# Performance work log

Hardware: AMD Instinct MI355X
Metric: run time of the kernel (lower is better)

## Reference

```python
import jax, jax.numpy as jnp
import numpy as np

MOLS = 64
ATOMS = 256
N = MOLS * ATOMS
K_GB = 32
K_GNN = 16
HID = 128
OFFSET = 0.009            # GB dielectric offset (nm)
ALPHA, BETA, GAMMA = 1.0, 0.8, 4.85  # OBC2 coefficients
EPS_FACTOR = 138.935456   # Coulomb constant, kJ*nm/(mol*e^2)
PREF = -EPS_FACTOR * (1.0 - 1.0 / 78.5)


def _edges(key, k_neigh):
    # random intra-molecule neighbors, no self loops (mimics radius-graph structure)
    src = jnp.repeat(jnp.arange(N), k_neigh)
    off = jax.random.randint(key, (N * k_neigh,), 1, ATOMS)
    dst = (src // ATOMS) * ATOMS + (src % ATOMS + off) % ATOMS
    return jnp.stack([src, dst]).astype(jnp.int32)


def setup_inputs() -> dict:
    key = jax.random.key(0)
    ks = jax.random.split(key, 8)
    pos = (jax.random.uniform(ks[0], (N, 3), jnp.float32) * 1.5)
    q = jax.random.uniform(ks[1], (N, 1), jnp.float32) - 0.5
    rad = 0.15 + 0.05 * jax.random.uniform(ks[2], (N, 1), jnp.float32)
    scl = 0.8 + 0.2 * jax.random.uniform(ks[3], (N, 1), jnp.float32)
    rest = jax.random.uniform(ks[4], (N, 4), jnp.float32)
    atom_features = jnp.concatenate([q, rad, scl, rest], axis=1)
    batch = jnp.repeat(jnp.arange(MOLS), ATOMS).astype(jnp.int32)
    edge_index = _edges(ks[5], K_GB)
    gnn_edge_index = _edges(ks[6], K_GNN)

    def lin(k, fi, fo):
        return (jax.random.normal(k, (fi, fo), jnp.float32) / np.float32(np.sqrt(fi)),
                jnp.zeros((fo,), jnp.float32))
    kw = jax.random.split(ks[7], 6)
    i1_w1, i1_b1 = lin(kw[0], 2 * 2 + 1, HID)
    i1_w2, i1_b2 = lin(kw[1], HID, HID)
    i2_w1, i2_b1 = lin(kw[2], 2 * HID + 1, HID)
    i2_w2, i2_b2 = lin(kw[3], HID, HID)
    i3_w1, i3_b1 = lin(kw[4], 2 * HID + 1, HID)
    i3_w2, i3_b2 = lin(kw[5], HID, 1)
    return dict(pos=pos, atom_features=atom_features, batch=batch,
                edge_index=edge_index, gnn_edge_index=gnn_edge_index,
                i1_w1=i1_w1, i1_b1=i1_b1, i1_w2=i1_w2, i1_b2=i1_b2,
                i2_w1=i2_w1, i2_b1=i2_b1, i2_w2=i2_w2, i2_b2=i2_b2,
                i3_w1=i3_w1, i3_b1=i3_b1, i3_w2=i3_w2, i3_b2=i3_b2)


def _dist(pos, ei):
    d2 = jnp.sum((pos[ei[0]] - pos[ei[1]]) ** 2, axis=1)
    return jnp.sqrt(d2 + 1e-12)


def _gb_energies(pos, feats, ei):
    # GBNeck_interaction (Born radii via HCT descreening integral, OBC2 rescale)
    # followed by GBNeck_energies (pairwise GB + self energy), per-atom [N,1]
    n = pos.shape[0]
    src, dst = ei[0], ei[1]
    d = _dist(pos, ei)
    q, radius, scale = feats[:, 0], feats[:, 1], feats[:, 2]
    rho = radius - OFFSET
    sr_j = (scale * rho)[src]
    rho_i = rho[dst]
    U = d + sr_j
    L = jnp.maximum(rho_i, jnp.abs(d - sr_j))
    I = 0.5 * (1.0 / L - 1.0 / U
               + 0.25 * (d - sr_j ** 2 / d) * (1.0 / U ** 2 - 1.0 / L ** 2)
               + 0.5 * jnp.log(L / U) / d)
    I = jnp.where(rho_i < U, I, 0.0)
    Isum = jax.ops.segment_sum(I, dst, num_segments=n)
    psi = Isum * rho
    B = 1.0 / (1.0 / rho - jnp.tanh(ALPHA * psi - BETA * psi ** 2 + GAMMA * psi ** 3) / radius)
    Bi, Bj = B[dst], B[src]
    f_gb = jnp.sqrt(d ** 2 + Bi * Bj * jnp.exp(-d ** 2 / (4.0 * Bi * Bj)))
    e_pair = 0.5 * PREF * q[dst] * q[src] / f_gb  # 0.5: edges are double counted
    e = 0.5 * PREF * q ** 2 / B + jax.ops.segment_sum(e_pair, dst, num_segments=n)
    return e[:, None]


def _in_layer(x, ei, d, w1, b1, w2, b2):
    # IN_layer_all_swish_2pass: edge MLP on [x_i || x_j || d] + scatter-add
    n = x.shape[0]
    m = jnp.concatenate([x[ei[0]], x[ei[1]], d[:, None]], axis=1)
    h = jax.nn.silu(m @ w1 + b1)
    return jax.ops.segment_sum(h @ w2 + b2, ei[1], num_segments=n)


def _energies_all(pos, feats, ei, gei,
                  i1_w1, i1_b1, i1_w2, i1_b2,
                  i2_w1, i2_b1, i2_w2, i2_b2,
                  i3_w1, i3_b1, i3_w2, i3_b2):
    e_gb = _gb_energies(pos, feats, ei)
    d_gnn = _dist(pos, gei)
    x = jax.nn.silu(_in_layer(feats[:, :2], gei, d_gnn, i1_w1, i1_b1, i1_w2, i1_b2))
    x = jax.nn.silu(_in_layer(x, gei, d_gnn, i2_w1, i2_b1, i2_w2, i2_b2))
    x = _in_layer(x, gei, d_gnn, i3_w1, i3_b1, i3_w2, i3_b2)
    return e_gb + x


def reference(pos, atom_features, batch, edge_index, gnn_edge_index,
              i1_w1, i1_b1, i1_w2, i1_b2,
              i2_w1, i2_b1, i2_w2, i2_b2,
              i3_w1, i3_b1, i3_w2, i3_b2):
    ws = (i1_w1, i1_b1, i1_w2, i1_b2, i2_w1, i2_b1, i2_w2, i2_b2,
          i3_w1, i3_b1, i3_w2, i3_b2)
    efun = lambda p: _energies_all(p, atom_features, edge_index, gnn_edge_index, *ws)
    energies, vjp = jax.vjp(efun, pos)  # [N,1]
    (gpos,) = vjp(jnp.ones_like(energies))
    forces = -gpos
    energy = jax.ops.segment_sum(energies[:, 0], batch, num_segments=MOLS)[:, None]
    return energy, forces
```

## Files before the change

### kernel.cpp

```cpp
#include <hip/hip_runtime.h>
#include <hip/hip_bf16.h>

#define NATOMS 16384
#define MOLS   64
#define ATOMSM 256
#define EGB    524288
#define EGNN   262144
#define HID    128
#define NH     (NATOMS*HID)

#define OFFSETC 0.009f
#define ALPHAC  1.0f
#define BETAC   0.8f
#define GAMMAC  4.85f
#define PREFC   (-138.935456f*(1.0f-1.0f/78.5f))

typedef __hip_bfloat16 bf;
typedef __attribute__((ext_vector_type(8))) short bf8v;
typedef __attribute__((ext_vector_type(4))) float f4v;

__device__ __forceinline__ float b2f(bf x){ return __bfloat162float(x); }
__device__ __forceinline__ bf f2b(float x){ return __float2bfloat16(x); }
__device__ __forceinline__ short f2s(float x){ bf h = f2b(x); return *(short*)&h; }
__device__ __forceinline__ float s2f(short s){
    unsigned int x = ((unsigned int)(unsigned short)s) << 16;
    return __uint_as_float(x);
}
__device__ __forceinline__ float sigf(float x){ return 1.0f/(1.0f+__expf(-x)); }
__device__ __forceinline__ float waveRed(float v){
    v += __shfl_xor(v,32); v += __shfl_xor(v,16); v += __shfl_xor(v,8);
    v += __shfl_xor(v,4);  v += __shfl_xor(v,2);  v += __shfl_xor(v,1);
    return v;
}

__global__ __launch_bounds__(256) void k_gbA_dist(
    const float* __restrict__ pos, const float* __restrict__ feat,
    const int* __restrict__ ei, float* __restrict__ Isum,
    const int* __restrict__ gei, float* __restrict__ dgnn, int* __restrict__ cnt)
{
    int tid = threadIdx.x;
    if (blockIdx.x < 512){
        __shared__ float sPx[256], sPy[256], sPz[256], sRho[256], sSr[256];
        __shared__ float sI[256];
        int mbase = (blockIdx.x >> 3) * 256;
        {
            int i = mbase + tid;
            sPx[tid]=pos[3*i]; sPy[tid]=pos[3*i+1]; sPz[tid]=pos[3*i+2];
            float rad = feat[7*i+1], sc = feat[7*i+2];
            float rho = rad - OFFSETC;
            sRho[tid]=rho; sSr[tid]=sc*rho;
            sI[tid]=0.f;
        }
        __syncthreads();
        int T = blockIdx.x*256 + tid;
        int s = T >> 3, p = T & 7;
        int sl = s & 255;
        int e0 = s*32 + p*4;
        float px = sPx[sl], py = sPy[sl], pz = sPz[sl];
        float sr = sSr[sl];
        const int* dP = ei + EGB;
#pragma unroll
        for (int j=0;j<4;j++){
            int dl = dP[e0+j] & 255;
            float dx = px - sPx[dl];
            float dy = py - sPy[dl];
            float dz = pz - sPz[dl];
            float d  = sqrtf(dx*dx+dy*dy+dz*dz + 1e-12f);
            float rho_i = sRho[dl];
            float U = d + sr;
            if (rho_i < U){
                float L = fmaxf(rho_i, fabsf(d - sr));
                float invU = 1.0f/U, invL = 1.0f/L;
                float I = 0.5f*invL - 0.5f*invU
                        + 0.125f*(d - sr*sr/d)*(invU*invU - invL*invL)
                        + 0.25f*__logf(L*invU)/d;
                atomicAdd(&sI[dl], I);
            }
        }
        __syncthreads();
        atomicAdd(&Isum[mbase + tid], sI[tid]);
    } else {
        int e = (blockIdx.x-512)*256 + tid;
        if (e >= EGNN) return;
        int s = gei[e], dd = gei[EGNN+e];
        float dx = pos[3*s+0] - pos[3*dd+0];
        float dy = pos[3*s+1] - pos[3*dd+1];
        float dz = pos[3*s+2] - pos[3*dd+2];
        dgnn[e] = sqrtf(dx*dx+dy*dy+dz*dz + 1e-12f);
        atomicAdd(&cnt[dd], 1);
    }
}

__global__ __launch_bounds__(256) void k_gbB_scan(
    const float* __restrict__ feat, const float* __restrict__ Isum,
    float* __restrict__ Bv, float* __restrict__ cB, float* __restrict__ gB,
    float* __restrict__ egb,
    const int* __restrict__ cnt, int* __restrict__ rptr, int* __restrict__ cursor)
{
    int t = threadIdx.x;
    if (blockIdx.x < 64){
        int i = blockIdx.x*256 + t;
        float q   = feat[7*i+0];
        float rad = feat[7*i+1];
        float rho = rad - OFFSETC;
        float psi = Isum[i]*rho;
        float u = psi*(ALPHAC + psi*(-BETAC + GAMMAC*psi));
        float tt = tanhf(u);
        float B = 1.0f/(1.0f/rho - tt/rad);
        Bv[i] = B;
        float du = ALPHAC + psi*(-2.0f*BETAC + 3.0f*GAMMAC*psi);
        cB[i] = B*B*((1.0f-tt*tt)/rad)*du*rho;
        float Cs = 0.5f*PREFC*q*q;
        egb[i] = Cs/B;
        gB[i]  = -Cs/(B*B);
    } else {
        __shared__ int sc[256];
        int m = blockIdx.x - 64;
        int c = cnt[m*256+t];
        sc[t] = c; __syncthreads();
        for (int off=1; off<256; off<<=1){
            int x = (t>=off) ? sc[t-off] : 0;
            __syncthreads();
            sc[t] += x;
            __syncthreads();
        }
        int ex = m*4096 + sc[t] - c;
        rptr[m*256+t] = ex;
        cursor[m*256+t] = ex;
    }
}

__global__ __launch_bounds__(256) void k_gbC(
    const float* __restrict__ pos, const float* __restrict__ feat,
    const int* __restrict__ ei, const float* __restrict__ Bv,
    float* __restrict__ egb, float* __restrict__ gdgb, float* __restrict__ gB)
{
    __shared__ float sPx[256], sPy[256], sPz[256], sB[256], sQf[256];
    __shared__ float sE[256], sG[256];
    int tid = threadIdx.x;
    int mbase = (blockIdx.x >> 3) * 256;
    {
        int i = mbase + tid;
        sPx[tid]=pos[3*i]; sPy[tid]=pos[3*i+1]; sPz[tid]=pos[3*i+2];
        sB[tid]=Bv[i]; sQf[tid]=feat[7*i+0];
        sE[tid]=0.f; sG[tid]=0.f;
    }
    __syncthreads();
    int T = blockIdx.x*256 + tid;
    int s = T >> 3, p = T & 7;
    int sl = s & 255;
    int e0 = s*32 + p*4;
    float px = sPx[sl], py = sPy[sl], pz = sPz[sl];
    float qs = sQf[sl];
    float Bs = sB[sl];
    float gsrc = 0.f;
    const int* dP = ei + EGB;
#pragma unroll
    for (int j=0;j<4;j++){
        int dl = dP[e0+j] & 255;
        float dx = px - sPx[dl];
        float dy = py - sPy[dl];
        float dz = pz - sPz[dl];
        float d2 = dx*dx+dy*dy+dz*dz + 1e-12f;
        float d  = sqrtf(d2);
        float Bd = sB[dl];
        float C = 0.5f*PREFC*sQf[dl]*qs;
        float P = Bd*Bs;
        float ex = __expf(-d2/(4.f*P));
        float f2 = d2 + P*ex;
        float f  = sqrtf(f2);
        float f3i = 1.f/(f2*f);
        gdgb[e0+j] = -C*d*(1.f - 0.25f*ex)*f3i;
        float common = -C*ex*(1.f + d2/(4.f*P))*0.5f*f3i;
        atomicAdd(&sE[dl], C/f);
        atomicAdd(&sG[dl], common*Bs);
        gsrc += common*Bd;
    }
    gsrc += __shfl_xor(gsrc,1);
    gsrc += __shfl_xor(gsrc,2);
    gsrc += __shfl_xor(gsrc,4);
    if (p==0) atomicAdd(&sG[sl], gsrc);
    __syncthreads();
    atomicAdd(&egb[mbase + tid], sE[tid]);
    atomicAdd(&gB[mbase + tid],  sG[tid]);
}

__global__ __launch_bounds__(256) void k_gbE(
    const float* __restrict__ pos, const float* __restrict__ feat,
    const int* __restrict__ ei, const float* __restrict__ cB,
    const float* __restrict__ gB,
    const float* __restrict__ gdgb, float* __restrict__ grad)
{
    __shared__ float sPx[256], sPy[256], sPz[256], sRho[256], sSr[256], sCg[256];
    __shared__ float sGx[256], sGy[256], sGz[256];
    int tid = threadIdx.x;
    int mbase = (blockIdx.x >> 3) * 256;
    {
        int i = mbase + tid;
        sPx[tid]=pos[3*i]; sPy[tid]=pos[3*i+1]; sPz[tid]=pos[3*i+2];
        float rad = feat[7*i+1], sc = feat[7*i+2];
        float rho = rad - OFFSETC;
        sRho[tid]=rho; sSr[tid]=sc*rho;
        sCg[tid]=cB[i]*gB[i];
        sGx[tid]=0.f; sGy[tid]=0.f; sGz[tid]=0.f;
    }
    __syncthreads();
    int T = blockIdx.x*256 + tid;
    int s = T >> 3, p = T & 7;
    int sl = s & 255;
    int e0 = s*32 + p*4;
    float px = sPx[sl], py = sPy[sl], pz = sPz[sl];
    float sr = sSr[sl];
    float gx=0.f, gy=0.f, gz=0.f;
    const int* dP = ei + EGB;
#pragma unroll
    for (int j=0;j<4;j++){
        int dl = dP[e0+j] & 255;
        float dx = px - sPx[dl];
        float dy = py - sPy[dl];
        float dz = pz - sPz[dl];
        float d2 = dx*dx+dy*dy+dz*dz + 1e-12f;
        float d  = sqrtf(d2);
        float rho_i = sRho[dl];
        float U = d + sr;
        float gd = gdgb[e0+j];
        if (rho_i < U){
            float aa = fabsf(d - sr);
            float L, Lp;
            if (rho_i >= aa){ L = rho_i; Lp = 0.f; }
            else { L = aa; Lp = (d >= sr) ? 1.f : -1.f; }
            float invU = 1.f/U, invL = 1.f/L;
            float invU2=invU*invU, invL2=invL*invL;
            float dIdd = -0.5f*Lp*invL2 + 0.5f*invU2
                + 0.125f*(1.f + sr*sr/d2)*(invU2 - invL2)
                + 0.125f*(d - sr*sr/d)*(2.f*Lp*invL2*invL - 2.f*invU2*invU)
                + 0.25f*((Lp*invL - invU)/d - __logf(L*invU)/d2);
            gd += sCg[dl]*dIdd;
        }
        float c = gd/d;
        gx += c*dx; gy += c*dy; gz += c*dz;
        atomicAdd(&sGx[dl], -c*dx);
        atomicAdd(&sGy[dl], -c*dy);
        atomicAdd(&sGz[dl], -c*dz);
    }
    gx += __shfl_xor(gx,1); gx += __shfl_xor(gx,2); gx += __shfl_xor(gx,4);
    gy += __shfl_xor(gy,1); gy += __shfl_xor(gy,2); gy += __shfl_xor(gy,4);
    gz += __shfl_xor(gz,1); gz += __shfl_xor(gz,2); gz += __shfl_xor(gz,4);
    if (p==0){
        atomicAdd(&sGx[sl], gx);
        atomicAdd(&sGy[sl], gy);
        atomicAdd(&sGz[sl], gz);
    }
    __syncthreads();
    int i = mbase + tid;
    atomicAdd(&grad[3*i+0], sGx[tid]);
    atomicAdd(&grad[3*i+1], sGy[tid]);
    atomicAdd(&grad[3*i+2], sGz[tid]);
}

__global__ __launch_bounds__(256) void k_fill(
    const int* __restrict__ gei, int* __restrict__ cursor, int* __restrict__ csr)
{
    int e = blockIdx.x*256 + threadIdx.x;
    if (e >= EGNN) return;
    int dst = gei[EGNN+e];
    int pos = atomicAdd(&cursor[dst], 1);
    csr[pos] = e;
}

__global__ __launch_bounds__(256) void k_pre(
    const float* __restrict__ A2, const float* __restrict__ C1,
    const float* __restrict__ A3, const float* __restrict__ C2,
    short* __restrict__ C1t, short* __restrict__ C2t,
    short* __restrict__ A2at, short* __restrict__ A2bt,
    short* __restrict__ A3at, short* __restrict__ A3bt,
    short* __restrict__ rA2a, short* __restrict__ rA2b,
    short* __restrict__ rA3a, short* __restrict__ rA3b,
    short* __restrict__ rC1, short* __restrict__ rC2,
    const float* __restrict__ feat, const float* __restrict__ A1,
    bf* __restrict__ u1, bf* __restrict__ v1)
{
    if (blockIdx.x < 64){
        int gid = blockIdx.x*256 + threadIdx.x;
        int j = gid >> 7, k = gid & 127;
        C1t[gid]  = f2s(C1[k*HID+j]);
        C2t[gid]  = f2s(C2[k*HID+j]);
        A2at[gid] = f2s(A2[k*HID+j]);
        A2bt[gid] = f2s(A2[(HID+k)*HID+j]);
        A3at[gid] = f2s(A3[k*HID+j]);
        A3bt[gid] = f2s(A3[(HID+k)*HID+j]);
        rA2a[gid] = f2s(A2[gid]);
        rA2b[gid] = f2s(A2[HID*HID+gid]);
        rA3a[gid] = f2s(A3[gid]);
        rA3b[gid] = f2s(A3[HID*HID+gid]);
        rC1[gid]  = f2s(C1[gid]);
        rC2[gid]  = f2s(C2[gid]);
    } else {
        int gid = (blockIdx.x-64)*256 + threadIdx.x;
        int i = gid >> 7, k = gid & 127;
        float q = feat[7*i+0], r = feat[7*i+1];
        u1[gid] = f2b(q*A1[k]       + r*A1[HID+k]);
        v1[gid] = f2b(q*A1[2*HID+k] + r*A1[3*HID+k]);
    }
}

__global__ __launch_bounds__(128) void k_edge_fwd_dst(
    const int* __restrict__ csr, const int* __restrict__ rptr, const int* __restrict__ cnt,
    const float* __restrict__ dgnn, const bf* __restrict__ u, const bf* __restrict__ v,
    const float* __restrict__ wdp, const float* __restrict__ bb,
    bf* __restrict__ Hs, bf* __restrict__ dsO, bf* __restrict__ Sds)
{
    int dst = blockIdx.x, k = threadIdx.x;
    int n = cnt[dst], r0 = rptr[dst];
    float wd = wdp[k];
    float base = b2f(v[dst*HID+k]) + bb[k];
    float hsum = 0.f, dssum = 0.f;
    const short* us = (const short*)u;
    short* dso = (short*)dsO;
#pragma unroll 2
    for (int j=0;j<n;j++){
        int e = csr[r0+j];
        float a = s2f(us[(size_t)(e>>4)*HID + k]) + base + dgnn[e]*wd;
        float sg = sigf(a);
        hsum += a*sg;
        float dv = sg*(1.f + a*(1.f - sg));
        dssum += dv;
        dso[(size_t)e*HID + k] = f2s(dv);
    }
    Hs[dst*HID+k] = f2b(hsum);
    Sds[dst*HID+k] = f2b(dssum);
}

__global__ __launch_bounds__(256) void k_node_fwd_uv_mfma(
    const short* __restrict__ Hs, const int* __restrict__ cnt,
    const short* __restrict__ Ct, const float* __restrict__ D,
    const short* __restrict__ Aat, const short* __restrict__ Abt,
    bf* __restrict__ dsz, bf* __restrict__ u, bf* __restrict__ v)
{
    __shared__ short sx[64*HID];
    int lane = threadIdx.x & 63, w = threadIdx.x >> 6;
    int m0 = blockIdx.x*64 + w*16;
    int ar = lane & 15, kg = lane >> 4;
    bf8v af[4];
#pragma unroll
    for (int s=0;s<4;s++) af[s] = *(const bf8v*)&Hs[(size_t)(m0+ar)*HID + s*32 + kg*8];
    f4v acc[8];
#pragma unroll
    for (int nt=0;nt<8;nt++){
        acc[nt] = (f4v){0.f,0.f,0.f,0.f};
        const short* bp = Ct + (nt*16+ar)*HID + kg*8;
#pragma unroll
        for (int s=0;s<4;s++){
            bf8v bv = *(const bf8v*)(bp + s*32);
            acc[nt] = __builtin_amdgcn_mfma_f32_16x16x32_bf16(af[s], bv, acc[nt], 0,0,0);
        }
    }
    float cn[4];
#pragma unroll
    for (int r=0;r<4;r++) cn[r] = (float)cnt[m0 + kg*4 + r];
#pragma unroll
    for (int nt=0;nt<8;nt++){
        int j = nt*16 + ar;
        float Dj = D[j];
#pragma unroll
        for (int r=0;r<4;r++){
            int m = m0 + kg*4 + r;
            float zv = acc[nt][r] + cn[r]*Dj;
            float sg = sigf(zv);
            dsz[(size_t)m*HID + j] = f2b(sg*(1.f + zv*(1.f - sg)));
            sx[(w*16 + kg*4 + r)*HID + j] = f2s(zv*sg);
        }
    }
    __syncthreads();
#pragma unroll
    for (int s=0;s<4;s++) af[s] = *(const bf8v*)&sx[(w*16+ar)*HID + s*32 + kg*8];
    f4v au[8], av[8];
#pragma unroll
    for (int nt=0;nt<8;nt++){
        au[nt] = (f4v){0.f,0.f,0.f,0.f};
        av[nt] = (f4v){0.f,0.f,0.f,0.f};
        const short* bpa = Aat + (nt*16+ar)*HID + kg*8;
        const short* bpb = Abt + (nt*16+ar)*HID + kg*8;
#pragma unroll
        for (int s=0;s<4;s++){
            bf8v ba = *(const bf8v*)(bpa + s*32);
            bf8v bb = *(const bf8v*)(bpb + s*32);
            au[nt] = __builtin_amdgcn_mfma_f32_16x16x32_bf16(af[s], ba, au[nt], 0,0,0);
            av[nt] = __builtin_amdgcn_mfma_f32_16x16x32_bf16(af[s], bb, av[nt], 0,0,0);
        }
    }
#pragma unroll
    for (int nt=0;nt<8;nt++){
        int j = nt*16 + ar;
#pragma unroll
        for (int r=0;r<4;r++){
            int m = m0 + kg*4 + r;
            u[(size_t)m*HID + j] = f2b(au[nt][r]);
            v[(size_t)m*HID + j] = f2b(av[nt][r]);
        }
    }
}

__global__ __launch_bounds__(256) void k_gx_node_bwd_mfma(
    const short* __restrict__ Gs, const short* __restrict__ Gd,
    const short* __restrict__ gHin, const short* __restrict__ Sds,
    const short* __restrict__ Ra, const short* __restrict__ Rb,
    const bf* __restrict__ dsz, const short* __restrict__ Rc,
    bf* __restrict__ gHout)
{
    __shared__ short st[64*HID];
    int lane = threadIdx.x & 63, w = threadIdx.x >> 6;
    int m0 = blockIdx.x*64 + w*16;
    int ar = lane & 15, kg = lane >> 4;
    bf8v as_[4], ad_[4];
#pragma unroll
    for (int s=0;s<4;s++)
        as_[s] = *(const bf8v*)&Gs[(size_t)(m0+ar)*HID + s*32 + kg*8];
    if (Sds){
#pragma unroll
        for (int s=0;s<4;s++){
            bf8v g = *(const bf8v*)&gHin[(size_t)(m0+ar)*HID + s*32 + kg*8];
            bf8v sd = *(const bf8v*)&Sds[(size_t)(m0+ar)*HID + s*32 + kg*8];
            bf8v r;
#pragma unroll
            for (int i=0;i<8;i++) r[i] = f2s(s2f(g[i])*s2f(sd[i]));
            ad_[s] = r;
        }
    } else {
#pragma unroll
        for (int s=0;s<4;s++)
            ad_[s] = *(const bf8v*)&Gd[(size_t)(m0+ar)*HID + s*32 + kg*8];
    }
    f4v acc[8];
#pragma unroll
    for (int nt=0;nt<8;nt++){
        acc[nt] = (f4v){0.f,0.f,0.f,0.f};
        const short* bpa = Ra + (nt*16+ar)*HID + kg*8;
        const short* bpb = Rb + (nt*16+ar)*HID + kg*8;
#pragma unroll
        for (int s=0;s<4;s++){
            bf8v ba = *(const bf8v*)(bpa + s*32);
            bf8v bb = *(const bf8v*)(bpb + s*32);
            acc[nt] = __builtin_amdgcn_mfma_f32_16x16x32_bf16(as_[s], ba, acc[nt], 0,0,0);
            acc[nt] = __builtin_amdgcn_mfma_f32_16x16x32_bf16(ad_[s], bb, acc[nt], 0,0,0);
        }
    }
#pragma unroll
    for (int nt=0;nt<8;nt++){
        int j = nt*16 + ar;
#pragma unroll
        for (int r=0;r<4;r++){
            int m = m0 + kg*4 + r;
            float t = acc[nt][r] * b2f(dsz[(size_t)m*HID + j]);
            st[(w*16 + kg*4 + r)*HID + j] = f2s(t);
        }
    }
    __syncthreads();
    bf8v af[4];
#pragma unroll
    for (int s=0;s<4;s++) af[s] = *(const bf8v*)&st[(w*16+ar)*HID + s*32 + kg*8];
    f4v a2[8];
#pragma unroll
    for (int nt=0;nt<8;nt++){
        a2[nt] = (f4v){0.f,0.f,0.f,0.f};
        const short* bp = Rc + (nt*16+ar)*HID + kg*8;
#pragma unroll
        for (int s=0;s<4;s++){
            bf8v bc = *(const bf8v*)(bp + s*32);
            a2[nt] = __builtin_amdgcn_mfma_f32_16x16x32_bf16(af[s], bc, a2[nt], 0,0,0);
        }
    }
#pragma unroll
    for (int nt=0;nt<8;nt++){
        int j = nt*16 + ar;
#pragma unroll
        for (int r=0;r<4;r++){
            gHout[(size_t)(m0 + kg*4 + r)*HID + j] = f2b(a2[nt][r]);
        }
    }
}

__global__ __launch_bounds__(128) void k_l3_dst(
    const int* __restrict__ csr, const int* __restrict__ rptr, const int* __restrict__ cnt,
    const float* __restrict__ dgnn, const bf* __restrict__ u, const bf* __restrict__ v,
    const float* __restrict__ A3, const float* __restrict__ B3,
    const float* __restrict__ C3, const float* __restrict__ D3,
    bf* __restrict__ ds3, bf* __restrict__ Gd, float* __restrict__ x3)
{
    __shared__ float rr[2];
    int dst = blockIdx.x, k = threadIdx.x;
    int n = cnt[dst], r0 = rptr[dst];
    float wd = A3[256*HID+k], ck = C3[k];
    float base = b2f(v[dst*HID+k]) + B3[k];
    float hsum = 0.f, dssum = 0.f;
    const short* us = (const short*)u;
    short* dso = (short*)ds3;
#pragma unroll 2
    for (int j=0;j<n;j++){
        int e = csr[r0+j];
        float a = s2f(us[(size_t)(e>>4)*HID + k]) + base + dgnn[e]*wd;
        float sg = sigf(a);
        hsum += a*sg;
        float dv = sg*(1.f + a*(1.f - sg));
        dssum += dv;
        dso[(size_t)e*HID + k] = f2s(dv);
    }
    Gd[dst*HID+k] = f2b(ck*dssum);
    float pv = waveRed(ck*hsum);
    if ((k&63)==0) rr[k>>6] = pv;
    __syncthreads();
    if (k==0) x3[dst] = rr[0] + rr[1] + (float)n*D3[0];
}

__global__ __launch_bounds__(128) void k_l3_src(
    const bf* __restrict__ ds3,
    const float* __restrict__ A3, const float* __restrict__ C3,
    bf* __restrict__ Gs, float* __restrict__ gdg)
{
    __shared__ short sds[2048];
    __shared__ float sQ[16][130];
    int s = blockIdx.x, k = threadIdx.x;
    const bf8v* slab = (const bf8v*)((const short*)ds3 + (size_t)s*2048);
    ((bf8v*)sds)[k]     = slab[k];
    ((bf8v*)sds)[128+k] = slab[128+k];
    __syncthreads();
    float wd = A3[256*HID+k], ck = C3[k];
    float cw = ck*wd;
    float gs = 0.f;
#pragma unroll
    for (int t=0;t<16;t++){
        float dv = s2f(sds[t*128+k]);
        gs += dv;
        sQ[t][k] = dv*cw;
    }
    Gs[s*HID+k] = f2b(ck*gs);
    __syncthreads();
    int t = k >> 3, r = k & 7;
    float pg = 0.f;
#pragma unroll
    for (int i=0;i<16;i++) pg += sQ[t][i + 16*r];
    pg += __shfl_xor(pg,1); pg += __shfl_xor(pg,2); pg += __shfl_xor(pg,4);
    if (r==0) gdg[s*16+t] = pg;
}

__global__ __launch_bounds__(128) void k_bwd_src(
    const int* __restrict__ gei, const bf* __restrict__ ds2,
    const float* __restrict__ wdp, const bf* __restrict__ gH,
    bf* __restrict__ Gs, float* __restrict__ gdg)
{
    __shared__ short sds[2048];
    __shared__ short sgh[2048];
    __shared__ float sQ[16][130];
    int s = blockIdx.x, k = threadIdx.x;
    const bf8v* slab = (const bf8v*)((const short*)ds2 + (size_t)s*2048);
    ((bf8v*)sds)[k]     = slab[k];
    ((bf8v*)sds)[128+k] = slab[128+k];
    {
        int t = k >> 3, q = k & 7;
        int dst = gei[EGNN + s*16 + t];
        const bf8v* gr = (const bf8v*)((const short*)gH + (size_t)dst*HID);
        ((bf8v*)sgh)[t*16 + q*2]     = gr[q*2];
        ((bf8v*)sgh)[t*16 + q*2 + 1] = gr[q*2+1];
    }
    __syncthreads();
    float wd = wdp[k];
    float gs = 0.f;
#pragma unroll
    for (int t=0;t<16;t++){
        float ga = s2f(sgh[t*128+k]) * s2f(sds[t*128+k]);
        gs += ga;
        sQ[t][k] = ga*wd;
    }
    Gs[s*HID+k] = f2b(gs);
    __syncthreads();
    int t = k >> 3, r = k & 7;
    float pg = 0.f;
#pragma unroll
    for (int i=0;i<16;i++) pg += sQ[t][i + 16*r];
    pg += __shfl_xor(pg,1); pg += __shfl_xor(pg,2); pg += __shfl_xor(pg,4);
    if (r==0) gdg[s*16+t] += pg;
}

__global__ __launch_bounds__(128) void k_bwd1_src(
    const int* __restrict__ gei, const bf* __restrict__ ds1,
    const float* __restrict__ wdp, const bf* __restrict__ gH,
    float* __restrict__ gdg)
{
    __shared__ short sds[2048];
    __shared__ short sgh[2048];
    __shared__ float sQ[16][130];
    int s = blockIdx.x, k = threadIdx.x;
    const bf8v* slab = (const bf8v*)((const short*)ds1 + (size_t)s*2048);
    ((bf8v*)sds)[k]     = slab[k];
    ((bf8v*)sds)[128+k] = slab[128+k];
    {
        int t = k >> 3, q = k & 7;
        int dst = gei[EGNN + s*16 + t];
        const bf8v* gr = (const bf8v*)((const short*)gH + (size_t)dst*HID);
        ((bf8v*)sgh)[t*16 + q*2]     = gr[q*2];
        ((bf8v*)sgh)[t*16 + q*2 + 1] = gr[q*2+1];
    }
    __syncthreads();
    float wd = wdp[k];
#pragma unroll
    for (int t=0;t<16;t++){
        float ga = s2f(sgh[t*128+k]) * s2f(sds[t*128+k]);
        sQ[t][k] = ga*wd;
    }
    __syncthreads();
    int t = k >> 3, r = k & 7;
    float pg = 0.f;
#pragma unroll
    for (int i=0;i<16;i++) pg += sQ[t][i + 16*r];
    pg += __shfl_xor(pg,1); pg += __shfl_xor(pg,2); pg += __shfl_xor(pg,4);
    if (r==0) gdg[s*16+t] += pg;
}

__global__ __launch_bounds__(256) void k_force_atom(
    const float* __restrict__ pos, const int* __restrict__ gei,
    const int* __restrict__ csr, const int* __restrict__ rptr, const int* __restrict__ cnt,
    const float* __restrict__ dgnn, const float* __restrict__ gdg,
    const float* __restrict__ grad, float* __restrict__ fout)
{
    int T = blockIdx.x*256 + threadIdx.x;
    int i = T >> 3, p = T & 7;
    float px = pos[3*i+0], py = pos[3*i+1], pz = pos[3*i+2];
    float ax=0.f, ay=0.f, az=0.f;
    for (int j=p;j<16;j+=8){
        int e = i*16 + j;
        int o = gei[EGNN+e];
        float c = gdg[e]/dgnn[e];
        ax += c*(px - pos[3*o+0]);
        ay += c*(py - pos[3*o+1]);
        az += c*(pz - pos[3*o+2]);
    }
    int n = cnt[i], r0 = rptr[i];
    for (int j=p;j<n;j+=8){
        int e = csr[r0+j];
        int o = e >> 4;
        float c = gdg[e]/dgnn[e];
        ax += c*(px - pos[3*o+0]);
        ay += c*(py - pos[3*o+1]);
        az += c*(pz - pos[3*o+2]);
    }
    ax += __shfl_xor(ax,1); ax += __shfl_xor(ax,2); ax += __shfl_xor(ax,4);
    ay += __shfl_xor(ay,1); ay += __shfl_xor(ay,2); ay += __shfl_xor(ay,4);
    az += __shfl_xor(az,1); az += __shfl_xor(az,2); az += __shfl_xor(az,4);
    if (p==0){
        fout[3*i+0] = -(grad[3*i+0] + ax);
        fout[3*i+1] = -(grad[3*i+1] + ay);
        fout[3*i+2] = -(grad[3*i+2] + az);
    }
}

__global__ __launch_bounds__(256) void k_final(
    const float* __restrict__ egb, const float* __restrict__ x3,
    float* __restrict__ out)
{
    __shared__ float red[4];
    int m = blockIdx.x, tid = threadIdx.x;
    int i = m*ATOMSM + tid;
    float en = egb[i] + x3[i];
    float v = waveRed(en);
    int wave = tid>>6, lane = tid&63;
    if (lane==0) red[wave] = v;
    __syncthreads();
    if (tid==0) out[m] = red[0]+red[1]+red[2]+red[3];
}

extern "C" void kernel_launch(void* const* d_in, const int* in_sizes, int n_in,
                              void* d_out, int out_size, void* d_ws, size_t ws_size,
                              hipStream_t stream)
{
    const float* pos  = (const float*)d_in[0];
    const float* feat = (const float*)d_in[1];
    const int* ei  = (const int*)d_in[3];
    const int* gei = (const int*)d_in[4];
    const float* A1f = (const float*)d_in[5];  const float* B1f = (const float*)d_in[6];
    const float* C1f = (const float*)d_in[7];  const float* D1f = (const float*)d_in[8];
    const float* A2f = (const float*)d_in[9];  const float* B2f = (const float*)d_in[10];
    const float* C2f = (const float*)d_in[11]; const float* D2f = (const float*)d_in[12];
    const float* A3f = (const float*)d_in[13]; const float* B3f = (const float*)d_in[14];
    const float* C3f = (const float*)d_in[15]; const float* D3f = (const float*)d_in[16];

    float* w = (float*)d_ws;
    size_t off = 0;
    auto nxt = [&](size_t n)->float*{ float* p = w + off; off += (n + 255) & ~(size_t)255; return p; };
    float* Isum = nxt(NATOMS);
    int*   cnt  = (int*)nxt(NATOMS);
    float* grad = nxt(3*NATOMS);
    float* Bv = nxt(NATOMS); float* cB = nxt(NATOMS);
    float* gB = nxt(NATOMS); float* egb = nxt(NATOMS); float* x3 = nxt(NATOMS);
    int*   rptr = (int*)nxt(NATOMS);
    int*   curs = (int*)nxt(NATOMS);
    int*   csr  = (int*)nxt(EGNN);
    float* dgnn = nxt(EGNN); float* gdgnn = nxt(EGNN); float* gdgb = nxt(EGB);
    bf* dsz1 = (bf*)nxt(NH/2); bf* dsz2 = (bf*)nxt(NH/2);
    bf* Hs1 = (bf*)nxt(NH/2); bf* Hs2 = (bf*)nxt(NH/2);
    bf* Gs3 = (bf*)nxt(NH/2); bf* Gd3 = (bf*)nxt(NH/2);
    bf* Sds2 = (bf*)nxt(NH/2);
    bf* u1 = (bf*)nxt(NH/2); bf* v1 = (bf*)nxt(NH/2);
    bf* u2 = (bf*)nxt(NH/2); bf* v2 = (bf*)nxt(NH/2);
    bf* v3 = (bf*)nxt(NH/2);
    short* C1t  = (short*)nxt(8192); short* C2t  = (short*)nxt(8192);
    short* A2at = (short*)nxt(8192); short* A2bt = (short*)nxt(8192);
    short* A3at = (short*)nxt(8192); short* A3bt = (short*)nxt(8192);
    short* rA2a = (short*)nxt(8192); short* rA2b = (short*)nxt(8192);
    short* rA3a = (short*)nxt(8192); short* rA3b = (short*)nxt(8192);
    short* rC1  = (short*)nxt(8192); short* rC2  = (short*)nxt(8192);
    bf* ds1 = (bf*)nxt((size_t)EGNN*HID/2);
    bf* ds2 = (bf*)nxt((size_t)EGNN*HID/2);
    bf* ds3 = (bf*)nxt((size_t)EGNN*HID/2);
    bf* u3  = Hs1;
    bf* gH2 = Hs2;
    bf* Gs2 = Gs3;
    bf* gH1 = u3;

    hipMemsetAsync(Isum, 0, (size_t)5*NATOMS*sizeof(float), stream);

    k_pre<<<64+NH/256,256,0,stream>>>(A2f, C1f, A3f, C2f,
        C1t, C2t, A2at, A2bt, A3at, A3bt, rA2a, rA2b, rA3a, rA3b, rC1, rC2,
        feat, A1f, u1, v1);

    k_gbA_dist<<<512+EGNN/256,256,0,stream>>>(pos, feat, ei, Isum, gei, dgnn, cnt);
    k_gbB_scan<<<128,256,0,stream>>>(feat, Isum, Bv, cB, gB, egb, cnt, rptr, curs);
    k_fill<<<EGNN/256,256,0,stream>>>(gei, curs, csr);
    k_gbC<<<512,256,0,stream>>>(pos, feat, ei, Bv, egb, gdgb, gB);
    k_gbE<<<512,256,0,stream>>>(pos, feat, ei, cB, gB, gdgb, grad);

    k_edge_fwd_dst<<<NATOMS,128,0,stream>>>(csr, rptr, cnt, dgnn, u1, v1,
                                            A1f+4*HID, B1f, Hs1, ds1, Sds2 );
    k_node_fwd_uv_mfma<<<NATOMS/64,256,0,stream>>>((const short*)Hs1, cnt, C1t, D1f,
                                                   A2at, A2bt, dsz1, u2, v2);
    k_edge_fwd_dst<<<NATOMS,128,0,stream>>>(csr, rptr, cnt, dgnn, u2, v2,
                                            A2f+256*HID, B2f, Hs2, ds2, Sds2);
    k_node_fwd_uv_mfma<<<NATOMS/64,256,0,stream>>>((const short*)Hs2, cnt, C2t, D2f,
                                                   A3at, A3bt, dsz2, u3, v3);

    k_l3_dst<<<NATOMS,128,0,stream>>>(csr, rptr, cnt, dgnn, u3, v3,
                                      A3f, B3f, C3f, D3f, ds3, Gd3, x3);
    k_l3_src<<<NATOMS,128,0,stream>>>(ds3, A3f, C3f, Gs3, gdgnn);

    k_gx_node_bwd_mfma<<<NATOMS/64,256,0,stream>>>((const short*)Gs3, (const short*)Gd3,
        (const short*)nullptr, (const short*)nullptr, rA3a, rA3b, dsz2, rC2, gH2);
    k_bwd_src<<<NATOMS,128,0,stream>>>(gei, ds2, A2f+256*HID, gH2, Gs2, gdgnn);
    k_gx_node_bwd_mfma<<<NATOMS/64,256,0,stream>>>((const short*)Gs2, (const short*)nullptr,
        (const short*)gH2, (const short*)Sds2, rA2a, rA2b, dsz1, rC1, gH1);
    k_bwd1_src<<<NATOMS,128,0,stream>>>(gei, ds1, A1f+4*HID, gH1, gdgnn);

    k_force_atom<<<NATOMS*8/256,256,0,stream>>>(pos, gei, csr, rptr, cnt, dgnn, gdgnn,
                                                grad, (float*)d_out + MOLS);
    k_final<<<MOLS,256,0,stream>>>(egb, x3, (float*)d_out);
}
```

Baseline: 385.0 us.

## Recompute per-edge SiLU derivatives in source kernels instead of storing them

The destination-side edge kernels no longer write the per-edge, per-channel SiLU derivative tensors (three EGNN×HID bf16 buffers). Instead, the source-side backward kernels rebuild the pre-activation from u[src], a gathered v[dst], the bias and the edge distance, then recompute the derivative in place. This removes a large global write and read of the per-edge activations, and frees their memory. The cost is extra gathers of v rows and extra sigmoid arithmetic in the source kernels, and values now come from fp32 recompute instead of bf16-rounded stores.

Measured after the change: 388.7 us. About the same (+1.0%).

```diff
diff --git a/kernel.cpp b/kernel.cpp
--- a/kernel.cpp
+++ b/kernel.cpp
@@ -308,7 +308,7 @@
     const int* __restrict__ csr, const int* __restrict__ rptr, const int* __restrict__ cnt,
     const float* __restrict__ dgnn, const bf* __restrict__ u, const bf* __restrict__ v,
     const float* __restrict__ wdp, const float* __restrict__ bb,
-    bf* __restrict__ Hs, bf* __restrict__ dsO, bf* __restrict__ Sds)
+    bf* __restrict__ Hs, bf* __restrict__ Sds)
 {
     int dst = blockIdx.x, k = threadIdx.x;
     int n = cnt[dst], r0 = rptr[dst];
@@ -316,19 +316,16 @@
     float base = b2f(v[dst*HID+k]) + bb[k];
     float hsum = 0.f, dssum = 0.f;
     const short* us = (const short*)u;
-    short* dso = (short*)dsO;
 #pragma unroll 2
     for (int j=0;j<n;j++){
         int e = csr[r0+j];
         float a = s2f(us[(size_t)(e>>4)*HID + k]) + base + dgnn[e]*wd;
         float sg = sigf(a);
         hsum += a*sg;
-        float dv = sg*(1.f + a*(1.f - sg));
-        dssum += dv;
-        dso[(size_t)e*HID + k] = f2s(dv);
+        dssum += sg*(1.f + a*(1.f - sg));
     }
     Hs[dst*HID+k] = f2b(hsum);
-    Sds[dst*HID+k] = f2b(dssum);
+    if (Sds) Sds[dst*HID+k] = f2b(dssum);
 }
 
 __global__ __launch_bounds__(256) void k_node_fwd_uv_mfma(
@@ -485,7 +482,7 @@
     const float* __restrict__ dgnn, const bf* __restrict__ u, const bf* __restrict__ v,
     const float* __restrict__ A3, const float* __restrict__ B3,
     const float* __restrict__ C3, const float* __restrict__ D3,
-    bf* __restrict__ ds3, bf* __restrict__ Gd, float* __restrict__ x3)
+    bf* __restrict__ Gd, float* __restrict__ x3)
 {
     __shared__ float rr[2];
     int dst = blockIdx.x, k = threadIdx.x;
@@ -494,16 +491,13 @@
     float base = b2f(v[dst*HID+k]) + B3[k];
     float hsum = 0.f, dssum = 0.f;
     const short* us = (const short*)u;
-    short* dso = (short*)ds3;
 #pragma unroll 2
     for (int j=0;j<n;j++){
         int e = csr[r0+j];
         float a = s2f(us[(size_t)(e>>4)*HID + k]) + base + dgnn[e]*wd;
         float sg = sigf(a);
         hsum += a*sg;
-        float dv = sg*(1.f + a*(1.f - sg));
-        dssum += dv;
-        dso[(size_t)e*HID + k] = f2s(dv);
+        dssum += sg*(1.f + a*(1.f - sg));
     }
     Gd[dst*HID+k] = f2b(ck*dssum);
     float pv = waveRed(ck*hsum);
@@ -513,23 +507,34 @@
 }
 
 __global__ __launch_bounds__(128) void k_l3_src(
-    const bf* __restrict__ ds3,
-    const float* __restrict__ A3, const float* __restrict__ C3,
+    const int* __restrict__ gei, const float* __restrict__ dgnn,
+    const bf* __restrict__ u, const bf* __restrict__ v,
+    const float* __restrict__ A3, const float* __restrict__ B3,
+    const float* __restrict__ C3,
     bf* __restrict__ Gs, float* __restrict__ gdg)
 {
-    __shared__ short sds[2048];
+    __shared__ short sv[2048];
     __shared__ float sQ[16][130];
+    __shared__ float sd[16];
     int s = blockIdx.x, k = threadIdx.x;
-    const bf8v* slab = (const bf8v*)((const short*)ds3 + (size_t)s*2048);
-    ((bf8v*)sds)[k]     = slab[k];
-    ((bf8v*)sds)[128+k] = slab[128+k];
+    {
+        int t = k >> 3, q = k & 7;
+        int dst = gei[EGNN + s*16 + t];
+        const bf8v* vr = (const bf8v*)((const short*)v + (size_t)dst*HID);
+        ((bf8v*)sv)[t*16 + q*2]     = vr[q*2];
+        ((bf8v*)sv)[t*16 + q*2 + 1] = vr[q*2+1];
+    }
+    if (k < 16) sd[k] = dgnn[s*16+k];
     __syncthreads();
     float wd = A3[256*HID+k], ck = C3[k];
+    float ub = s2f(((const short*)u)[(size_t)s*HID+k]) + B3[k];
     float cw = ck*wd;
     float gs = 0.f;
 #pragma unroll
     for (int t=0;t<16;t++){
-        float dv = s2f(sds[t*128+k]);
+        float a = ub + s2f(sv[t*128+k]) + sd[t]*wd;
+        float sg = sigf(a);
+        float dv = sg*(1.f + a*(1.f - sg));
         gs += dv;
         sQ[t][k] = dv*cw;
     }
@@ -544,30 +549,38 @@
 }
 
 __global__ __launch_bounds__(128) void k_bwd_src(
-    const int* __restrict__ gei, const bf* __restrict__ ds2,
-    const float* __restrict__ wdp, const bf* __restrict__ gH,
+    const int* __restrict__ gei, const float* __restrict__ dgnn,
+    const bf* __restrict__ u, const bf* __restrict__ v,
+    const float* __restrict__ wdp, const float* __restrict__ bb,
+    const bf* __restrict__ gH,
     bf* __restrict__ Gs, float* __restrict__ gdg)
 {
-    __shared__ short sds[2048];
+    __shared__ short sv[2048];
     __shared__ short sgh[2048];
     __shared__ float sQ[16][130];
+    __shared__ float sd[16];
     int s = blockIdx.x, k = threadIdx.x;
-    const bf8v* slab = (const bf8v*)((const short*)ds2 + (size_t)s*2048);
-    ((bf8v*)sds)[k]     = slab[k];
-    ((bf8v*)sds)[128+k] = slab[128+k];
     {
         int t = k >> 3, q = k & 7;
         int dst = gei[EGNN + s*16 + t];
+        const bf8v* vr = (const bf8v*)((const short*)v + (size_t)dst*HID);
         const bf8v* gr = (const bf8v*)((const short*)gH + (size_t)dst*HID);
+        ((bf8v*)sv)[t*16 + q*2]      = vr[q*2];
+        ((bf8v*)sv)[t*16 + q*2 + 1]  = vr[q*2+1];
         ((bf8v*)sgh)[t*16 + q*2]     = gr[q*2];
         ((bf8v*)sgh)[t*16 + q*2 + 1] = gr[q*2+1];
     }
+    if (k < 16) sd[k] = dgnn[s*16+k];
     __syncthreads();
     float wd = wdp[k];
+    float ub = s2f(((const short*)u)[(size_t)s*HID+k]) + bb[k];
     float gs = 0.f;
 #pragma unroll
     for (int t=0;t<16;t++){
-        float ga = s2f(sgh[t*128+k]) * s2f(sds[t*128+k]);
+        float a = ub + s2f(sv[t*128+k]) + sd[t]*wd;
+        float sg = sigf(a);
+        float dv = sg*(1.f + a*(1.f - sg));
+        float ga = s2f(sgh[t*128+k]) * dv;
         gs += ga;
         sQ[t][k] = ga*wd;
     }
@@ -582,29 +595,37 @@
 }
 
 __global__ __launch_bounds__(128) void k_bwd1_src(
-    const int* __restrict__ gei, const bf* __restrict__ ds1,
-    const float* __restrict__ wdp, const bf* __restrict__ gH,
+    const int* __restrict__ gei, const float* __restrict__ dgnn,
+    const bf* __restrict__ u, const bf* __restrict__ v,
+    const float* __restrict__ wdp, const float* __restrict__ bb,
+    const bf* __restrict__ gH,
     float* __restrict__ gdg)
 {
-    __shared__ short sds[2048];
+    __shared__ short sv[2048];
     __shared__ short sgh[2048];
     __shared__ float sQ[16][130];
+    __shared__ float sd[16];
     int s = blockIdx.x, k = threadIdx.x;
-    const bf8v* slab = (const bf8v*)((const short*)ds1 + (size_t)s*2048);
-    ((bf8v*)sds)[k]     = slab[k];
-    ((bf8v*)sds)[128+k] = slab[128+k];
     {
         int t = k >> 3, q = k & 7;
         int dst = gei[EGNN + s*16 + t];
+        const bf8v* vr = (const bf8v*)((const short*)v + (size_t)dst*HID);
         const bf8v* gr = (const bf8v*)((const short*)gH + (size_t)dst*HID);
+        ((bf8v*)sv)[t*16 + q*2]      = vr[q*2];
+        ((bf8v*)sv)[t*16 + q*2 + 1]  = vr[q*2+1];
         ((bf8v*)sgh)[t*16 + q*2]     = gr[q*2];
         ((bf8v*)sgh)[t*16 + q*2 + 1] = gr[q*2+1];
     }
+    if (k < 16) sd[k] = dgnn[s*16+k];
     __syncthreads();
     float wd = wdp[k];
+    float ub = s2f(((const short*)u)[(size_t)s*HID+k]) + bb[k];
 #pragma unroll
     for (int t=0;t<16;t++){
-        float ga = s2f(sgh[t*128+k]) * s2f(sds[t*128+k]);
+        float a = ub + s2f(sv[t*128+k]) + sd[t]*wd;
+        float sg = sigf(a);
+        float dv = sg*(1.f + a*(1.f - sg));
+        float ga = s2f(sgh[t*128+k]) * dv;
         sQ[t][k] = ga*wd;
     }
     __syncthreads();
@@ -708,9 +729,6 @@
     short* rA2a = (short*)nxt(8192); short* rA2b = (short*)nxt(8192);
     short* rA3a = (short*)nxt(8192); short* rA3b = (short*)nxt(8192);
     short* rC1  = (short*)nxt(8192); short* rC2  = (short*)nxt(8192);
-    bf* ds1 = (bf*)nxt((size_t)EGNN*HID/2);
-    bf* ds2 = (bf*)nxt((size_t)EGNN*HID/2);
-    bf* ds3 = (bf*)nxt((size_t)EGNN*HID/2);
     bf* u3  = Hs1;
     bf* gH2 = Hs2;
     bf* Gs2 = Gs3;
@@ -729,24 +747,24 @@
     k_gbE<<<512,256,0,stream>>>(pos, feat, ei, cB, gB, gdgb, grad);
 
     k_edge_fwd_dst<<<NATOMS,128,0,stream>>>(csr, rptr, cnt, dgnn, u1, v1,
-                                            A1f+4*HID, B1f, Hs1, ds1, Sds2 );
+                                            A1f+4*HID, B1f, Hs1, (bf*)nullptr);
     k_node_fwd_uv_mfma<<<NATOMS/64,256,0,stream>>>((const short*)Hs1, cnt, C1t, D1f,
                                                    A2at, A2bt, dsz1, u2, v2);
     k_edge_fwd_dst<<<NATOMS,128,0,stream>>>(csr, rptr, cnt, dgnn, u2, v2,
-                                            A2f+256*HID, B2f, Hs2, ds2, Sds2);
+                                            A2f+256*HID, B2f, Hs2, Sds2);
     k_node_fwd_uv_mfma<<<NATOMS/64,256,0,stream>>>((const short*)Hs2, cnt, C2t, D2f,
                                                    A3at, A3bt, dsz2, u3, v3);
 
     k_l3_dst<<<NATOMS,128,0,stream>>>(csr, rptr, cnt, dgnn, u3, v3,
-                                      A3f, B3f, C3f, D3f, ds3, Gd3, x3);
-    k_l3_src<<<NATOMS,128,0,stream>>>(ds3, A3f, C3f, Gs3, gdgnn);
+                                      A3f, B3f, C3f, D3f, Gd3, x3);
+    k_l3_src<<<NATOMS,128,0,stream>>>(gei, dgnn, u3, v3, A3f, B3f, C3f, Gs3, gdgnn);
 
     k_gx_node_bwd_mfma<<<NATOMS/64,256,0,stream>>>((const short*)Gs3, (const short*)Gd3,
         (const short*)nullptr, (const short*)nullptr, rA3a, rA3b, dsz2, rC2, gH2);
-    k_bwd_src<<<NATOMS,128,0,stream>>>(gei, ds2, A2f+256*HID, gH2, Gs2, gdgnn);
+    k_bwd_src<<<NATOMS,128,0,stream>>>(gei, dgnn, u2, v2, A2f+256*HID, B2f, gH2, Gs2, gdgnn);
     k_gx_node_bwd_mfma<<<NATOMS/64,256,0,stream>>>((const short*)Gs2, (const short*)nullptr,
         (const short*)gH2, (const short*)Sds2, rA2a, rA2b, dsz1, rC1, gH1);
-    k_bwd1_src<<<NATOMS,128,0,stream>>>(gei, ds1, A1f+4*HID, gH1, gdgnn);
+    k_bwd1_src<<<NATOMS,128,0,stream>>>(gei, dgnn, u1, v1, A1f+4*HID, B1f, gH1, gdgnn);
 
     k_force_atom<<<NATOMS*8/256,256,0,stream>>>(pos, gei, csr, rptr, cnt, dgnn, gdgnn,
                                                 grad, (float*)d_out + MOLS);
```
